# Optimization experiments

Measured on AMD Instinct MI355X. Metric: run time of the kernel, lower is better.

The kernel has to match this reference:

```python
import jax, jax.numpy as jnp
import numpy as np

SCALES = (0.25, 0.125, 0.0625, 0.03125)
OUT = 7   # output_size
SR = 2    # sampling_ratio


def _to_rois(boxes):
    # boxes: [B, N, 4] -> rois: [B*N, 5] = (batch_id, x1, y1, x2, y2)
    B, N, _ = boxes.shape
    ids = jnp.broadcast_to(jnp.arange(B, dtype=boxes.dtype)[:, None, None], (B, N, 1))
    return jnp.concatenate([ids, boxes], axis=-1).reshape(B * N, 5)


def _roi_align(feat, rois, scale, out_size, sr):
    #   roi coords scaled by spatial_scale, roi w/h clamped to >= 1,
    #   sr x sr bilinear samples per output bin, averaged.
    B, C, H, W = feat.shape
    R = rois.shape[0]
    dt = feat.dtype
    bidx = rois[:, 0].astype(jnp.int32)
    x1 = rois[:, 1] * scale
    y1 = rois[:, 2] * scale
    x2 = rois[:, 3] * scale
    y2 = rois[:, 4] * scale
    rw = jnp.maximum(x2 - x1, 1.0)
    rh = jnp.maximum(y2 - y1, 1.0)
    # sample coordinate (k+0.5)/sr in units of bin size, k in [0, out_size*sr)
    g = (jnp.arange(out_size * sr, dtype=dt) + 0.5) / sr          # [PS]
    ys = y1[:, None] + (rh / out_size)[:, None] * g               # [R, PS]
    xs = x1[:, None] + (rw / out_size)[:, None] * g               # [R, PS]
    Hf = jnp.asarray(H, dt); Wf = jnp.asarray(W, dt)
    vy = (ys >= -1.0) & (ys <= Hf)                                # out-of-range -> 0
    vx = (xs >= -1.0) & (xs <= Wf)
    yc = jnp.clip(ys, 0.0, Hf - 1.0)
    xc = jnp.clip(xs, 0.0, Wf - 1.0)
    y0 = jnp.floor(yc).astype(jnp.int32)
    x0 = jnp.floor(xc).astype(jnp.int32)
    y1i = jnp.minimum(y0 + 1, H - 1)
    x1i = jnp.minimum(x0 + 1, W - 1)
    ly = yc - y0.astype(dt); lx = xc - x0.astype(dt)
    hy = 1.0 - ly; hx = 1.0 - lx
    b = bidx[:, None, None]                                       # [R,1,1]
    Y0 = y0[:, :, None]; Y1 = y1i[:, :, None]                     # [R,PS,1]
    X0 = x0[:, None, :]; X1 = x1i[:, None, :]                     # [R,1,PS]
    # advanced indexing with a middle slice -> [R, PS, PS, C]
    v00 = feat[b, :, Y0, X0]
    v01 = feat[b, :, Y0, X1]
    v10 = feat[b, :, Y1, X0]
    v11 = feat[b, :, Y1, X1]
    wy0 = hy[:, :, None, None]; wy1 = ly[:, :, None, None]
    wx0 = hx[:, None, :, None]; wx1 = lx[:, None, :, None]
    val = v00 * (wy0 * wx0) + v01 * (wy0 * wx1) + v10 * (wy1 * wx0) + v11 * (wy1 * wx1)
    valid = (vy[:, :, None] & vx[:, None, :])[..., None]
    val = jnp.where(valid, val, jnp.zeros((), dt))
    # average sr x sr samples per bin: [R, P, S, P, S, C] -> [R, P, P, C]
    val = val.reshape(R, out_size, sr, out_size, sr, C).mean(axis=(2, 4))
    return jnp.transpose(val, (0, 3, 1, 2))                       # [R, C, P, P]


def setup_inputs() -> dict:
    key = jax.random.key(0)
    ks = jax.random.split(key, 5)
    B, C, N = 2, 256, 512
    img_h, img_w = 800.0, 1216.0
    x0 = jax.random.normal(ks[0], (B, C, 200, 304), jnp.float32)
    x1 = jax.random.normal(ks[1], (B, C, 100, 152), jnp.float32)
    x2 = jax.random.normal(ks[2], (B, C, 50, 76), jnp.float32)
    x3 = jax.random.normal(ks[3], (B, C, 25, 38), jnp.float32)
    u = jax.random.uniform(ks[4], (B, N, 4), jnp.float32)
    bx1 = u[..., 0] * (img_w - 17.0)
    by1 = u[..., 1] * (img_h - 17.0)
    bw = 16.0 + u[..., 2] * 240.0
    bh = 16.0 + u[..., 3] * 240.0
    bx2 = jnp.minimum(bx1 + bw, img_w - 1.0)
    by2 = jnp.minimum(by1 + bh, img_h - 1.0)
    boxes = jnp.stack([bx1, by1, bx2, by2], axis=-1)
    return {"x0": x0, "x1": x1, "x2": x2, "x3": x3, "boxes": boxes}


def reference(x0, x1, x2, x3, boxes):
    rois = _to_rois(boxes)
    feats = (x0, x1, x2, x3)
    return tuple(_roi_align(f, rois, s, OUT, SR) for f, s in zip(feats, SCALES))
```

## Files before the change

kernel.cpp:

```cpp
#include <hip/hip_runtime.h>


#define OUTSZ 7
#define NBIN  49
#define NSAMP 196
#define ROI_STRIDE 12544u
#define LVL_STRIDE 12845056u

typedef float f2v __attribute__((ext_vector_type(2)));
typedef float f4v __attribute__((ext_vector_type(4)));

#define WS_BYTES 165376000ull

__global__ __launch_bounds__(256)
void nchw_to_nhwc(const float* __restrict__ src, float* __restrict__ dst, int HW)
{
    __shared__ float tile[64 * 257];
    const int t  = threadIdx.x;
    const int p0 = blockIdx.x * 64;
    const int b  = blockIdx.y;
    const float* s = src + (size_t)b * 256u * (size_t)HW;
    float* d       = dst + (size_t)b * (size_t)HW * 256u;

    const int pl4 = (t & 15) * 4;
    const int ch  = t >> 4;
    const int p   = p0 + pl4;

    #pragma unroll 1
    for (int cc = 0; cc < 16; ++cc) {
        const int c = cc * 16 + ch;
        if (p + 3 < HW) {
            const f4v v = *reinterpret_cast<const f4v*>(s + (size_t)c * HW + p);
            tile[(pl4 + 0) * 257 + c] = v.x;
            tile[(pl4 + 1) * 257 + c] = v.y;
            tile[(pl4 + 2) * 257 + c] = v.z;
            tile[(pl4 + 3) * 257 + c] = v.w;
        } else {
            for (int j = 0; j < 4; ++j)
                if (p + j < HW) tile[(pl4 + j) * 257 + c] = s[(size_t)c * HW + p + j];
        }
    }
    __syncthreads();

    #pragma unroll 1
    for (int i = 0; i < 64; ++i) {
        const int pp = p0 + i;
        if (pp < HW) d[(size_t)pp * 256u + t] = tile[i * 257 + t];
    }
}

__global__ __launch_bounds__(256)
void roi_gather_nhwc(const float* __restrict__ ws, const float* __restrict__ boxes,
                     float* __restrict__ out)
{
    __shared__ float obuf[NBIN * 257];

    const int r   = blockIdx.x;
    const int lvl = blockIdx.y;
    const int t   = threadIdx.x;
    const int wv  = t >> 6;
    const int l   = t & 63;

    int H, W; float scale; size_t off;
    switch (lvl) {
      case 0:  H = 200; W = 304; scale = 0.25f;    off = 0u;        break;
      case 1:  H = 100; W = 152; scale = 0.125f;   off = 31129600u; break;
      case 2:  H = 50;  W = 76;  scale = 0.0625f;  off = 38912000u; break;
      default: H = 25;  W = 38;  scale = 0.03125f; off = 40857600u; break;
    }
    const int HW = H * W;
    const int b  = r >> 9;
    const float* base = ws + off + (size_t)b * (size_t)HW * 256u;

    const float bx1 = boxes[r * 4 + 0] * scale;
    const float by1 = boxes[r * 4 + 1] * scale;
    const float bx2 = boxes[r * 4 + 2] * scale;
    const float by2 = boxes[r * 4 + 3] * scale;
    const float rw  = fmaxf(bx2 - bx1, 1.0f);
    const float rh  = fmaxf(by2 - by1, 1.0f);
    const float bw7 = rw * (1.0f / 7.0f);
    const float bh7 = rh * (1.0f / 7.0f);
    const float Hf = (float)H, Wf = (float)W;

    #pragma unroll 1
    for (int bin = wv; bin < NBIN; bin += 4) {
        const int ph = bin / 7;
        const int pw = bin - ph * 7;
        f4v acc = {0.0f, 0.0f, 0.0f, 0.0f};

        #pragma unroll
        for (int sub = 0; sub < 4; ++sub) {
            const int ky = 2 * ph + (sub >> 1);
            const int kx = 2 * pw + (sub & 1);
            const float ys = by1 + bh7 * (((float)ky + 0.5f) * 0.5f);
            const float xs = bx1 + bw7 * (((float)kx + 0.5f) * 0.5f);

            const bool vy = (ys >= -1.0f) && (ys <= Hf);
            const bool vx = (xs >= -1.0f) && (xs <= Wf);

            const float yc = fminf(fmaxf(ys, 0.0f), Hf - 1.0f);
            const float xc = fminf(fmaxf(xs, 0.0f), Wf - 1.0f);
            const int y0 = (int)yc;
            const int x0 = (int)xc;
            const int y1i = min(y0 + 1, H - 1);
            const float ly = yc - (float)y0, lx = xc - (float)x0;
            const float hy = 1.0f - ly, hx = 1.0f - lx;

            int px; float wxA, wxB;
            if (x0 < W - 1) { px = x0;     wxA = hx;   wxB = lx;   }
            else            { px = W - 2;  wxA = 0.0f; wxB = 1.0f; }

            const float vm  = (vy && vx) ? 0.25f : 0.0f;
            const float w00 = hy * wxA * vm;
            const float w01 = hy * wxB * vm;
            const float w10 = ly * wxA * vm;
            const float w11 = ly * wxB * vm;

            const float* r0 = base + (size_t)(y0  * W + px) * 256u;
            const float* r1 = base + (size_t)(y1i * W + px) * 256u;

            const f4v a0 = *reinterpret_cast<const f4v*>(r0 + 4 * l);
            const f4v b0 = *reinterpret_cast<const f4v*>(r0 + 256 + 4 * l);
            const f4v a1 = *reinterpret_cast<const f4v*>(r1 + 4 * l);
            const f4v b1 = *reinterpret_cast<const f4v*>(r1 + 256 + 4 * l);

            acc += a0 * w00 + b0 * w01 + a1 * w10 + b1 * w11;
        }

        const int s = bin * 257 + 4 * l;
        obuf[s + 0] = acc.x;
        obuf[s + 1] = acc.y;
        obuf[s + 2] = acc.z;
        obuf[s + 3] = acc.w;
    }
    __syncthreads();

    float* o = out + (size_t)lvl * LVL_STRIDE + (size_t)r * ROI_STRIDE;
    #pragma unroll 1
    for (int k = 0; k < NBIN; ++k) {
        const int item = k * 256 + t;
        const unsigned c = (unsigned)item / 49u;
        const int bin = item - (int)c * 49;
        o[item] = obuf[bin * 257 + (int)c];
    }
}

__device__ __forceinline__ f2v load_f2(const float* p) {
    f2v v; __builtin_memcpy(&v, p, 8); return v;
}

__global__ __launch_bounds__(256)
void roi_align_all_levels(const float* __restrict__ f0,
                          const float* __restrict__ f1,
                          const float* __restrict__ f2,
                          const float* __restrict__ f3,
                          const float* __restrict__ boxes,
                          float* __restrict__ out)
{
    __shared__ int   sD0[NSAMP];
    __shared__ int   sD1[NSAMP];
    __shared__ float sW0[NSAMP];
    __shared__ float sW1[NSAMP];
    __shared__ float sW2[NSAMP];
    __shared__ float sW3[NSAMP];

    const int r   = blockIdx.x;
    const int lvl = blockIdx.y;
    const int t   = threadIdx.x;

    int H, W; float scale; const float* feat;
    switch (lvl) {
      case 0:  H = 200; W = 304; scale = 0.25f;    feat = f0; break;
      case 1:  H = 100; W = 152; scale = 0.125f;   feat = f1; break;
      case 2:  H = 50;  W = 76;  scale = 0.0625f;  feat = f2; break;
      default: H = 25;  W = 38;  scale = 0.03125f; feat = f3; break;
    }
    const unsigned HW = (unsigned)(H * W);
    const int b = r >> 9;

    if (t < NSAMP) {
        const float bx1 = boxes[r * 4 + 0] * scale;
        const float by1 = boxes[r * 4 + 1] * scale;
        const float bx2 = boxes[r * 4 + 2] * scale;
        const float by2 = boxes[r * 4 + 3] * scale;
        const float rw  = fmaxf(bx2 - bx1, 1.0f);
        const float rh  = fmaxf(by2 - by1, 1.0f);

        const int bin = t >> 2, sub = t & 3;
        const int ph = bin / 7, pw = bin % 7;
        const int ky = 2 * ph + (sub >> 1);
        const int kx = 2 * pw + (sub & 1);

        const float gy = ((float)ky + 0.5f) * 0.5f;
        const float gx = ((float)kx + 0.5f) * 0.5f;
        const float ys = by1 + (rh / 7.0f) * gy;
        const float xs = bx1 + (rw / 7.0f) * gx;

        const float Hf = (float)H, Wf = (float)W;
        const bool vy = (ys >= -1.0f) && (ys <= Hf);
        const bool vx = (xs >= -1.0f) && (xs <= Wf);

        const float yc = fminf(fmaxf(ys, 0.0f), Hf - 1.0f);
        const float xc = fminf(fmaxf(xs, 0.0f), Wf - 1.0f);
        const int y0 = (int)yc;
        const int x0 = (int)xc;
        const int y1i = min(y0 + 1, H - 1);
        const float ly = yc - (float)y0, lx = xc - (float)x0;
        const float hy = 1.0f - ly, hx = 1.0f - lx;

        int px; float wxA, wxB;
        if (x0 < W - 1) { px = x0;     wxA = hx;   wxB = lx;   }
        else            { px = W - 2;  wxA = 0.0f; wxB = 1.0f; }

        const float vm = (vy && vx) ? 0.25f : 0.0f;

        const int s = sub * NBIN + bin;
        sD0[s] = y0  * W + px;
        sD1[s] = y1i * W + px;
        sW0[s] = hy * wxA * vm;
        sW1[s] = hy * wxB * vm;
        sW2[s] = ly * wxA * vm;
        sW3[s] = ly * wxB * vm;
    }
    __syncthreads();

    const float* base = feat + (size_t)b * (size_t)(256u * HW);
    float* o = out + (size_t)lvl * LVL_STRIDE + (size_t)r * ROI_STRIDE;

    #pragma unroll 1
    for (int i = 0; i < 48; i += 2) {
        const int itemA = i * 256 + t;
        const int itemB = itemA + 256;
        const unsigned cA = (unsigned)itemA / 49u;
        const unsigned cB = (unsigned)itemB / 49u;
        const int binA = itemA - (int)cA * 49;
        const int binB = itemB - (int)cB * 49;
        const float* pA = base + (size_t)cA * HW;
        const float* pB = base + (size_t)cB * HW;

        float accA = 0.0f, accB = 0.0f;
        #pragma unroll
        for (int sub = 0; sub < 4; ++sub) {
            const int sA = sub * NBIN + binA;
            const int sB = sub * NBIN + binB;
            const f2v a0 = load_f2(pA + sD0[sA]);
            const f2v a1 = load_f2(pA + sD1[sA]);
            const f2v b0 = load_f2(pB + sD0[sB]);
            const f2v b1 = load_f2(pB + sD1[sB]);
            accA += a0.x * sW0[sA] + a0.y * sW1[sA]
                  + a1.x * sW2[sA] + a1.y * sW3[sA];
            accB += b0.x * sW0[sB] + b0.y * sW1[sB]
                  + b1.x * sW2[sB] + b1.y * sW3[sB];
        }
        o[itemA] = accA;
        o[itemB] = accB;
    }
    {
        const int item = 48 * 256 + t;
        const unsigned c = (unsigned)item / 49u;
        const int bin = item - (int)c * 49;
        const float* p = base + (size_t)c * HW;
        float acc = 0.0f;
        #pragma unroll
        for (int sub = 0; sub < 4; ++sub) {
            const int s = sub * NBIN + bin;
            const f2v a0 = load_f2(p + sD0[s]);
            const f2v a1 = load_f2(p + sD1[s]);
            acc += a0.x * sW0[s] + a0.y * sW1[s]
                 + a1.x * sW2[s] + a1.y * sW3[s];
        }
        o[item] = acc;
    }
}

extern "C" void kernel_launch(void* const* d_in, const int* in_sizes, int n_in,
                              void* d_out, int out_size, void* d_ws, size_t ws_size,
                              hipStream_t stream) {
    const float* f0    = (const float*)d_in[0];
    const float* f1    = (const float*)d_in[1];
    const float* f2    = (const float*)d_in[2];
    const float* f3    = (const float*)d_in[3];
    const float* boxes = (const float*)d_in[4];
    float* out = (float*)d_out;

    if (d_ws != nullptr && ws_size >= WS_BYTES) {
        float* w = (float*)d_ws;
        nchw_to_nhwc<<<dim3(950, 2), 256, 0, stream>>>(f0, w + 0u,        60800);
        nchw_to_nhwc<<<dim3(238, 2), 256, 0, stream>>>(f1, w + 31129600u, 15200);
        nchw_to_nhwc<<<dim3(60,  2), 256, 0, stream>>>(f2, w + 38912000u, 3800);
        nchw_to_nhwc<<<dim3(15,  2), 256, 0, stream>>>(f3, w + 40857600u, 950);
        roi_gather_nhwc<<<dim3(1024, 4), 256, 0, stream>>>(w, boxes, out);
    } else {
        dim3 grid(1024, 4);
        roi_align_all_levels<<<grid, 256, 0, stream>>>(f0, f1, f2, f3, boxes, out);
    }
}
```

Measured before the change: 533.6 us.

## Fuse transpose launches, precompute sample tables, split gather by channel halves

The four NCHW-to-NHWC transpose launches are merged into one launch that dispatches by block index. It uses 32-pixel tiles and vectorized float4 stores from shared memory. The ROI gather kernel now computes the 196 sample offsets and weights once per block into shared memory instead of in every wave. It also splits the 256 channels across two blocks per ROI and level, giving twice the blocks and a smaller shared buffer, at the cost of 8-byte loads and duplicated sample setup.

```diff
diff --git a/kernel.cpp b/kernel.cpp
--- a/kernel.cpp
+++ b/kernel.cpp
@@ -13,39 +13,56 @@
 #define WS_BYTES 165376000ull
 
 __global__ __launch_bounds__(256)
-void nchw_to_nhwc(const float* __restrict__ src, float* __restrict__ dst, int HW)
+void fused_to_nhwc(const float* __restrict__ f0, const float* __restrict__ f1,
+                   const float* __restrict__ f2, const float* __restrict__ f3,
+                   float* __restrict__ ws)
 {
-    __shared__ float tile[64 * 257];
+    __shared__ __align__(16) float tile[32 * 260];
+    const int bx = blockIdx.x;
+    const int b  = blockIdx.y;
     const int t  = threadIdx.x;
-    const int p0 = blockIdx.x * 64;
-    const int b  = blockIdx.y;
-    const float* s = src + (size_t)b * 256u * (size_t)HW;
-    float* d       = dst + (size_t)b * (size_t)HW * 256u;
-
-    const int pl4 = (t & 15) * 4;
-    const int ch  = t >> 4;
-    const int p   = p0 + pl4;
-
-    #pragma unroll 1
-    for (int cc = 0; cc < 16; ++cc) {
-        const int c = cc * 16 + ch;
-        if (p + 3 < HW) {
-            const f4v v = *reinterpret_cast<const f4v*>(s + (size_t)c * HW + p);
-            tile[(pl4 + 0) * 257 + c] = v.x;
-            tile[(pl4 + 1) * 257 + c] = v.y;
-            tile[(pl4 + 2) * 257 + c] = v.z;
-            tile[(pl4 + 3) * 257 + c] = v.w;
+
+    const float* src; float* dst; int HW; int pb;
+    if (bx < 1900)      { src = f0; dst = ws;             HW = 60800; pb = bx; }
+    else if (bx < 2375) { src = f1; dst = ws + 31129600u; HW = 15200; pb = bx - 1900; }
+    else if (bx < 2494) { src = f2; dst = ws + 38912000u; HW = 3800;  pb = bx - 2375; }
+    else                { src = f3; dst = ws + 40857600u; HW = 950;   pb = bx - 2494; }
+
+    src += (size_t)b * 256u * (size_t)HW;
+    dst += (size_t)b * (size_t)HW * 256u;
+
+    const int p0 = pb * 32;
+    const int pg = (t & 7) * 4;
+    const int cb = t >> 3;
+
+    #pragma unroll
+    for (int i = 0; i < 8; ++i) {
+        const int c   = i * 32 + cb;
+        const int pos = p0 + pg;
+        const float* sp = src + (size_t)c * HW + pos;
+        if (pos + 3 < HW) {
+            f4v v; __builtin_memcpy(&v, sp, 16);
+            tile[(pg + 0) * 260 + c] = v.x;
+            tile[(pg + 1) * 260 + c] = v.y;
+            tile[(pg + 2) * 260 + c] = v.z;
+            tile[(pg + 3) * 260 + c] = v.w;
         } else {
+            #pragma unroll
             for (int j = 0; j < 4; ++j)
-                if (p + j < HW) tile[(pl4 + j) * 257 + c] = s[(size_t)c * HW + p + j];
+                if (pos + j < HW) tile[(pg + j) * 260 + c] = sp[j];
         }
     }
     __syncthreads();
 
-    #pragma unroll 1
-    for (int i = 0; i < 64; ++i) {
-        const int pp = p0 + i;
-        if (pp < HW) d[(size_t)pp * 256u + t] = tile[i * 257 + t];
+    const int wv = t >> 6, l = t & 63;
+    #pragma unroll
+    for (int i = 0; i < 8; ++i) {
+        const int pl = i * 4 + wv;
+        const int pp = p0 + pl;
+        if (pp < HW) {
+            const f4v v = *reinterpret_cast<const f4v*>(&tile[pl * 260 + 4 * l]);
+            *reinterpret_cast<f4v*>(dst + (size_t)pp * 256u + 4 * l) = v;
+        }
     }
 }
 
@@ -53,13 +70,15 @@
 void roi_gather_nhwc(const float* __restrict__ ws, const float* __restrict__ boxes,
                      float* __restrict__ out)
 {
-    __shared__ float obuf[NBIN * 257];
-
-    const int r   = blockIdx.x;
-    const int lvl = blockIdx.y;
-    const int t   = threadIdx.x;
-    const int wv  = t >> 6;
-    const int l   = t & 63;
+    __shared__ int   sO0[NSAMP], sO1[NSAMP];
+    __shared__ float sW0[NSAMP], sW1[NSAMP], sW2[NSAMP], sW3[NSAMP];
+    __shared__ float obuf[NBIN * 129];
+
+    const int r     = blockIdx.x;
+    const int lvl   = blockIdx.y;
+    const int chalf = blockIdx.z;
+    const int t  = threadIdx.x;
+    const int wv = t >> 6, l = t & 63;
 
     int H, W; float scale; size_t off;
     switch (lvl) {
@@ -70,78 +89,87 @@
     }
     const int HW = H * W;
     const int b  = r >> 9;
-    const float* base = ws + off + (size_t)b * (size_t)HW * 256u;
-
-    const float bx1 = boxes[r * 4 + 0] * scale;
-    const float by1 = boxes[r * 4 + 1] * scale;
-    const float bx2 = boxes[r * 4 + 2] * scale;
-    const float by2 = boxes[r * 4 + 3] * scale;
-    const float rw  = fmaxf(bx2 - bx1, 1.0f);
-    const float rh  = fmaxf(by2 - by1, 1.0f);
-    const float bw7 = rw * (1.0f / 7.0f);
-    const float bh7 = rh * (1.0f / 7.0f);
-    const float Hf = (float)H, Wf = (float)W;
+
+    if (t < NSAMP) {
+        const float bx1 = boxes[r * 4 + 0] * scale;
+        const float by1 = boxes[r * 4 + 1] * scale;
+        const float bx2 = boxes[r * 4 + 2] * scale;
+        const float by2 = boxes[r * 4 + 3] * scale;
+        const float rw  = fmaxf(bx2 - bx1, 1.0f);
+        const float rh  = fmaxf(by2 - by1, 1.0f);
+
+        const int bin = t >> 2, sub = t & 3;
+        const int ph = bin / 7, pw = bin % 7;
+        const int ky = 2 * ph + (sub >> 1);
+        const int kx = 2 * pw + (sub & 1);
+
+        const float ys = by1 + (rh * (1.0f / 7.0f)) * (((float)ky + 0.5f) * 0.5f);
+        const float xs = bx1 + (rw * (1.0f / 7.0f)) * (((float)kx + 0.5f) * 0.5f);
+
+        const float Hf = (float)H, Wf = (float)W;
+        const bool vy = (ys >= -1.0f) && (ys <= Hf);
+        const bool vx = (xs >= -1.0f) && (xs <= Wf);
+
+        const float yc = fminf(fmaxf(ys, 0.0f), Hf - 1.0f);
+        const float xc = fminf(fmaxf(xs, 0.0f), Wf - 1.0f);
+        const int y0 = (int)yc;
+        const int x0 = (int)xc;
+        const int y1i = min(y0 + 1, H - 1);
+        const float ly = yc - (float)y0, lx = xc - (float)x0;
+        const float hy = 1.0f - ly, hx = 1.0f - lx;
+
+        int px; float wxA, wxB;
+        if (x0 < W - 1) { px = x0;     wxA = hx;   wxB = lx;   }
+        else            { px = W - 2;  wxA = 0.0f; wxB = 1.0f; }
+
+        const float vm = (vy && vx) ? 0.25f : 0.0f;
+
+        sO0[t] = (y0  * W + px) * 256;
+        sO1[t] = (y1i * W + px) * 256;
+        sW0[t] = hy * wxA * vm;
+        sW1[t] = hy * wxB * vm;
+        sW2[t] = ly * wxA * vm;
+        sW3[t] = ly * wxB * vm;
+    }
+    __syncthreads();
+
+    const float* base = ws + off + (size_t)b * (size_t)HW * 256u
+                         + (size_t)(chalf * 128 + 2 * l);
 
     #pragma unroll 1
     for (int bin = wv; bin < NBIN; bin += 4) {
-        const int ph = bin / 7;
-        const int pw = bin - ph * 7;
-        f4v acc = {0.0f, 0.0f, 0.0f, 0.0f};
-
+        f2v acc = {0.0f, 0.0f};
         #pragma unroll
         for (int sub = 0; sub < 4; ++sub) {
-            const int ky = 2 * ph + (sub >> 1);
-            const int kx = 2 * pw + (sub & 1);
-            const float ys = by1 + bh7 * (((float)ky + 0.5f) * 0.5f);
-            const float xs = bx1 + bw7 * (((float)kx + 0.5f) * 0.5f);
-
-            const bool vy = (ys >= -1.0f) && (ys <= Hf);
-            const bool vx = (xs >= -1.0f) && (xs <= Wf);
-
-            const float yc = fminf(fmaxf(ys, 0.0f), Hf - 1.0f);
-            const float xc = fminf(fmaxf(xs, 0.0f), Wf - 1.0f);
-            const int y0 = (int)yc;
-            const int x0 = (int)xc;
-            const int y1i = min(y0 + 1, H - 1);
-            const float ly = yc - (float)y0, lx = xc - (float)x0;
-            const float hy = 1.0f - ly, hx = 1.0f - lx;
-
-            int px; float wxA, wxB;
-            if (x0 < W - 1) { px = x0;     wxA = hx;   wxB = lx;   }
-            else            { px = W - 2;  wxA = 0.0f; wxB = 1.0f; }
-
-            const float vm  = (vy && vx) ? 0.25f : 0.0f;
-            const float w00 = hy * wxA * vm;
-            const float w01 = hy * wxB * vm;
-            const float w10 = ly * wxA * vm;
-            const float w11 = ly * wxB * vm;
-
-            const float* r0 = base + (size_t)(y0  * W + px) * 256u;
-            const float* r1 = base + (size_t)(y1i * W + px) * 256u;
-
-            const f4v a0 = *reinterpret_cast<const f4v*>(r0 + 4 * l);
-            const f4v b0 = *reinterpret_cast<const f4v*>(r0 + 256 + 4 * l);
-            const f4v a1 = *reinterpret_cast<const f4v*>(r1 + 4 * l);
-            const f4v b1 = *reinterpret_cast<const f4v*>(r1 + 256 + 4 * l);
-
+            const int s = bin * 4 + sub;
+            const int o0 = sO0[s], o1 = sO1[s];
+            const float w00 = sW0[s], w01 = sW1[s], w10 = sW2[s], w11 = sW3[s];
+            f2v a0, b0, a1, b1;
+            __builtin_memcpy(&a0, base + o0,       8);
+            __builtin_memcpy(&b0, base + o0 + 256, 8);
+            __builtin_memcpy(&a1, base + o1,       8);
+            __builtin_memcpy(&b1, base + o1 + 256, 8);
             acc += a0 * w00 + b0 * w01 + a1 * w10 + b1 * w11;
         }
-
-        const int s = bin * 257 + 4 * l;
-        obuf[s + 0] = acc.x;
-        obuf[s + 1] = acc.y;
-        obuf[s + 2] = acc.z;
-        obuf[s + 3] = acc.w;
+        obuf[bin * 129 + 2 * l]     = acc.x;
+        obuf[bin * 129 + 2 * l + 1] = acc.y;
     }
     __syncthreads();
 
-    float* o = out + (size_t)lvl * LVL_STRIDE + (size_t)r * ROI_STRIDE;
+    float* o = out + (size_t)lvl * LVL_STRIDE + (size_t)r * ROI_STRIDE
+                   + (size_t)chalf * 6272u;
     #pragma unroll 1
-    for (int k = 0; k < NBIN; ++k) {
+    for (int k = 0; k < 24; ++k) {
         const int item = k * 256 + t;
         const unsigned c = (unsigned)item / 49u;
         const int bin = item - (int)c * 49;
-        o[item] = obuf[bin * 257 + (int)c];
+        o[item] = obuf[bin * 129 + (int)c];
+    }
+    if (t < 128) {
+        const int item = 6144 + t;
+        const unsigned c = (unsigned)item / 49u;
+        const int bin = item - (int)c * 49;
+        o[item] = obuf[bin * 129 + (int)c];
     }
 }
 
@@ -285,11 +313,8 @@
 
     if (d_ws != nullptr && ws_size >= WS_BYTES) {
         float* w = (float*)d_ws;
-        nchw_to_nhwc<<<dim3(950, 2), 256, 0, stream>>>(f0, w + 0u,        60800);
-        nchw_to_nhwc<<<dim3(238, 2), 256, 0, stream>>>(f1, w + 31129600u, 15200);
-        nchw_to_nhwc<<<dim3(60,  2), 256, 0, stream>>>(f2, w + 38912000u, 3800);
-        nchw_to_nhwc<<<dim3(15,  2), 256, 0, stream>>>(f3, w + 40857600u, 950);
-        roi_gather_nhwc<<<dim3(1024, 4), 256, 0, stream>>>(w, boxes, out);
+        fused_to_nhwc<<<dim3(2524, 2), 256, 0, stream>>>(f0, f1, f2, f3, w);
+        roi_gather_nhwc<<<dim3(1024, 4, 2), 256, 0, stream>>>(w, boxes, out);
     } else {
         dim3 grid(1024, 4);
         roi_align_all_levels<<<grid, 256, 0, stream>>>(f0, f1, f2, f3, boxes, out);
```

Measured after the change: 538.4 us. No clear change (+0.9%).
